# Kernel tuning notes

Measured on AMD Instinct MI355X. Metric: run time of the kernel, lower is better.

## Reference

```python
import jax, jax.numpy as jnp
import numpy as np

IN_F = 4096
OUT_F = 11008
GROUP_SIZE = 128
BITS = 4
PACK = 32 // BITS  # 8 uint4 nibbles per int32


def _unpack_uint4(packed):
    # packed: (rows, cols) int32 -> (rows, cols*8) int32 nibbles in [0,15]
    shifts = (jnp.arange(PACK, dtype=jnp.int32) * BITS)[None, None, :]
    nib = (packed[:, :, None] >> shifts) & 15
    return nib.reshape(packed.shape[0], packed.shape[1] * PACK)


def _dequant(qweight, qzeros, scales):
    # Mirrors torch.ops.hpu.convert_from_uint4: w = (uint4 - zp) * scale,
    # group-wise along the in_features dimension (rows).
    w = _unpack_uint4(qweight).astype(scales.dtype)          # (IN_F, OUT_F)
    zp = _unpack_uint4(qzeros).astype(scales.dtype)          # (n_groups, OUT_F)
    sc_full = jnp.repeat(scales, GROUP_SIZE, axis=0)          # (IN_F, OUT_F)
    zp_full = jnp.repeat(zp, GROUP_SIZE, axis=0)              # (IN_F, OUT_F)
    return (w - zp_full) * sc_full


def setup_inputs() -> dict:
    key = jax.random.key(0)
    k1, k2, k3, k4 = jax.random.split(key, 4)
    n_groups = IN_F // GROUP_SIZE
    inp = jax.random.normal(k1, (2, 2048, IN_F), dtype=jnp.float32)
    qweight = jax.random.randint(k2, (IN_F, OUT_F // PACK), 0, 2147483647, dtype=jnp.int32)
    qzeros = jax.random.randint(k3, (n_groups, OUT_F // PACK), 0, 2147483647, dtype=jnp.int32)
    scales = jax.random.uniform(k4, (n_groups, OUT_F), dtype=jnp.float32) * 0.01 + 1e-3
    return {"input": inp, "qweight": qweight, "qzeros": qzeros, "scales": scales}


def reference(input, qweight, qzeros, scales):
    weight = _dequant(qweight, qzeros, scales)                # (IN_F, OUT_F)
    out = jnp.einsum('bsi,io->bso', input, weight)            # (B, S, OUT_F)
    return out.astype(input.dtype)
```

## Files before the change

kernel.cpp:

```cpp
#include <hip/hip_runtime.h>
#include <stdint.h>

#define IN_F   4096
#define OUT_F  11008
#define QCOLS  (OUT_F / 8)
#define NGRP   32
#define M_TOT  4096

typedef __attribute__((ext_vector_type(8))) short short8;
typedef __attribute__((ext_vector_type(4))) float floatx4;

__device__ __forceinline__ short f2bf(float f) {
    union { float f; uint32_t u; } v; v.f = f;
    uint32_t u = v.u;
    u += 0x7FFFu + ((u >> 16) & 1u);
    return (short)(u >> 16);
}

__global__ __launch_bounds__(256)
void dequant_kernel(const int* __restrict__ qw, const int* __restrict__ qz,
                    const float* __restrict__ scl, short* __restrict__ wt)
{
    __shared__ int qlds[64 * 32];

    const int tid = threadIdx.x;
    const int nb  = blockIdx.x;
    const int kb  = blockIdx.y;
    const int n0  = nb * 256;
    const int c0  = nb * 32;
    const int k0  = kb * 64;
    const int g   = kb >> 1;

    #pragma unroll
    for (int i = 0; i < 8; ++i) {
        const int f = tid + i * 256;
        const int k = f >> 5, c = f & 31;
        qlds[f] = qw[(size_t)(k0 + k) * QCOLS + c0 + c];
    }
    __syncthreads();

    const int   cl = tid >> 3;
    const int   sh = (tid & 7) << 2;
    const uint32_t z  = (uint32_t)qz[(size_t)g * QCOLS + c0 + cl];
    const float sc = scl[(size_t)g * OUT_F + n0 + tid];
    const float zo = -(float)((z >> sh) & 15u) * sc;

    short8 o[8];
    #pragma unroll
    for (int i = 0; i < 8; ++i) {
        #pragma unroll
        for (int kk = 0; kk < 8; ++kk) {
            const uint32_t q = (uint32_t)qlds[(i * 8 + kk) * 32 + cl];
            o[i][kk] = f2bf(fmaf((float)((q >> sh) & 15u), sc, zo));
        }
    }

    short* dst = wt + (size_t)(n0 + tid) * IN_F + k0;
    #pragma unroll
    for (int i = 0; i < 8; ++i)
        *(short8*)(dst + i * 8) = o[i];
}

__global__ __launch_bounds__(256)
void cast_kernel(const float* __restrict__ A, short* __restrict__ Ab)
{
    const size_t i = ((size_t)blockIdx.x * 256 + threadIdx.x) * 8;
    const float4 a0 = *(const float4*)(A + i);
    const float4 a1 = *(const float4*)(A + i + 4);
    short8 o;
    o[0] = f2bf(a0.x); o[1] = f2bf(a0.y); o[2] = f2bf(a0.z); o[3] = f2bf(a0.w);
    o[4] = f2bf(a1.x); o[5] = f2bf(a1.y); o[6] = f2bf(a1.z); o[7] = f2bf(a1.w);
    *(short8*)(Ab + i) = o;
}

#define GBK 64

__global__ __launch_bounds__(256, 3)
void gemm_kernel(const short* __restrict__ Ab, const short* __restrict__ Bt,
                 float* __restrict__ out)
{
    __shared__ short As[128 * GBK];
    __shared__ short Bs[128 * GBK];

    const int tid  = threadIdx.x;
    const int lane = tid & 63;
    const int w    = tid >> 6;
    const int m0   = blockIdx.x * 128;
    const int n0   = blockIdx.y * 128;

    const int srow = lane >> 3;
    const int kseg = (lane & 7) ^ srow;
    const short* agp[4];
    const short* bgp[4];
    short* alp[4];
    short* blp[4];
    #pragma unroll
    for (int s = 0; s < 4; ++s) {
        const int slot = w * 4 + s;
        const int row  = slot * 8 + srow;
        agp[s] = Ab + (size_t)(m0 + row) * IN_F + kseg * 8;
        bgp[s] = Bt + (size_t)(n0 + row) * IN_F + kseg * 8;
        alp[s] = As + slot * 512;
        blp[s] = Bs + slot * 512;
    }

    const int lrow = lane & 15;
    const int quad = lane >> 4;
    const int wm   = ((w >> 1) & 1) << 6;
    const int wn   = (w & 1) << 6;

    int aoff[4], boff[4];
    #pragma unroll
    for (int i = 0; i < 4; ++i) {
        const int swz = (quad ^ (lrow & 7)) * 8;
        aoff[i] = (wm + i * 16 + lrow) * GBK + swz;
        boff[i] = (wn + i * 16 + lrow) * GBK + swz;
    }

    floatx4 acc[4][4];
    #pragma unroll
    for (int i = 0; i < 4; ++i)
        #pragma unroll
        for (int j = 0; j < 4; ++j)
            acc[i][j] = (floatx4)0.f;

    for (int it = 0; it < IN_F / GBK; ++it) {
        __syncthreads();
        #pragma unroll
        for (int s = 0; s < 4; ++s) {
            __builtin_amdgcn_global_load_lds(
                (const __attribute__((address_space(1))) void*)agp[s],
                (__attribute__((address_space(3))) void*)alp[s], 16, 0, 0);
            __builtin_amdgcn_global_load_lds(
                (const __attribute__((address_space(1))) void*)bgp[s],
                (__attribute__((address_space(3))) void*)blp[s], 16, 0, 0);
            agp[s] += GBK;
            bgp[s] += GBK;
        }
        __syncthreads();

        #pragma unroll
        for (int kx = 0; kx < 64; kx += 32) {
            short8 af[4], bf[4];
            #pragma unroll
            for (int mt = 0; mt < 4; ++mt)
                af[mt] = *(const short8*)(As + (aoff[mt] ^ kx));
            #pragma unroll
            for (int nt = 0; nt < 4; ++nt)
                bf[nt] = *(const short8*)(Bs + (boff[nt] ^ kx));
            #pragma unroll
            for (int mt = 0; mt < 4; ++mt)
                #pragma unroll
                for (int nt = 0; nt < 4; ++nt)
                    acc[mt][nt] = __builtin_amdgcn_mfma_f32_16x16x32_bf16(
                        af[mt], bf[nt], acc[mt][nt], 0, 0, 0);
        }
    }

    #pragma unroll
    for (int mt = 0; mt < 4; ++mt) {
        #pragma unroll
        for (int nt = 0; nt < 4; ++nt) {
            const int col = n0 + wn + nt * 16 + lrow;
            float* op = out + (size_t)(m0 + wm + mt * 16 + quad * 4) * OUT_F + col;
            #pragma unroll
            for (int r = 0; r < 4; ++r)
                op[(size_t)r * OUT_F] = acc[mt][nt][r];
        }
    }
}

#define BM 128
#define BN 128
#define LDA 40
#define LDB 40

__global__ __launch_bounds__(256, 2)
void wql_kernel(const float* __restrict__ A,
                const int*   __restrict__ qw,
                const int*   __restrict__ qz,
                const float* __restrict__ scl,
                float*       __restrict__ out)
{
    __shared__ short As[BM * LDA];
    __shared__ short Bs[BN * LDB];

    const int tid = threadIdx.x;
    const int m0  = blockIdx.y * BM;
    const int n0  = blockIdx.x * BN;

    const int a_row  = tid >> 1;
    const int a_kseg = (tid & 1) << 4;
    const float* a_base = A + (size_t)(m0 + a_row) * IN_F + a_kseg;
    short* a_wr = &As[a_row * LDA + a_kseg];

    const int b_n     = tid & 127;
    const int b_khalf = (tid >> 7) << 4;
    const int c_glob  = (n0 >> 3) + (b_n >> 3);
    const int shift   = (b_n & 7) << 2;
    short* b_wr = &Bs[b_n * LDB + b_khalf];

    const int lane = tid & 63;
    const int wm   = ((tid >> 7) & 1) << 6;
    const int wn   = ((tid >> 6) & 1) << 6;
    const int lrow = lane & 15;
    const int quad = lane >> 4;

    const short* a_rd = &As[(wm + lrow) * LDA + quad * 8];
    const short* b_rd = &Bs[(wn + lrow) * LDB + quad * 8];

    floatx4 acc[4][4];
    #pragma unroll
    for (int i = 0; i < 4; ++i)
        #pragma unroll
        for (int j = 0; j < 4; ++j)
            acc[i][j] = (floatx4)0.f;

    for (int g = 0; g < NGRP; ++g) {
        const uint32_t z  = (uint32_t)qz[g * QCOLS + c_glob];
        const float    sc = scl[g * OUT_F + n0 + b_n];
        const float    zo = -(float)((z >> shift) & 15u) * sc;

        #pragma unroll 1
        for (int t4 = 0; t4 < 4; ++t4) {
            const int k0 = (g << 7) + (t4 << 5);
            const float4* ap = (const float4*)(a_base + k0);
            float4 av0 = ap[0], av1 = ap[1], av2 = ap[2], av3 = ap[3];

            const int* qp = qw + (size_t)(k0 + b_khalf) * QCOLS + c_glob;
            uint32_t qv[16];
            #pragma unroll
            for (int kk = 0; kk < 16; ++kk) qv[kk] = (uint32_t)qp[kk * QCOLS];

            __syncthreads();

            short8 aw0, aw1;
            aw0[0]=f2bf(av0.x); aw0[1]=f2bf(av0.y); aw0[2]=f2bf(av0.z); aw0[3]=f2bf(av0.w);
            aw0[4]=f2bf(av1.x); aw0[5]=f2bf(av1.y); aw0[6]=f2bf(av1.z); aw0[7]=f2bf(av1.w);
            aw1[0]=f2bf(av2.x); aw1[1]=f2bf(av2.y); aw1[2]=f2bf(av2.z); aw1[3]=f2bf(av2.w);
            aw1[4]=f2bf(av3.x); aw1[5]=f2bf(av3.y); aw1[6]=f2bf(av3.z); aw1[7]=f2bf(av3.w);
            *(short8*)a_wr       = aw0;
            *(short8*)(a_wr + 8) = aw1;

            short8 bw0, bw1;
            #pragma unroll
            for (int kk = 0; kk < 8; ++kk)
                bw0[kk] = f2bf(fmaf((float)((qv[kk] >> shift) & 15u), sc, zo));
            #pragma unroll
            for (int kk = 0; kk < 8; ++kk)
                bw1[kk] = f2bf(fmaf((float)((qv[8 + kk] >> shift) & 15u), sc, zo));
            *(short8*)b_wr       = bw0;
            *(short8*)(b_wr + 8) = bw1;

            __syncthreads();

            short8 af[4], bf[4];
            #pragma unroll
            for (int mt = 0; mt < 4; ++mt)
                af[mt] = *(const short8*)(a_rd + mt * 16 * LDA);
            #pragma unroll
            for (int nt = 0; nt < 4; ++nt)
                bf[nt] = *(const short8*)(b_rd + nt * 16 * LDB);

            #pragma unroll
            for (int mt = 0; mt < 4; ++mt)
                #pragma unroll
                for (int nt = 0; nt < 4; ++nt)
                    acc[mt][nt] = __builtin_amdgcn_mfma_f32_16x16x32_bf16(
                        af[mt], bf[nt], acc[mt][nt], 0, 0, 0);
        }
    }

    #pragma unroll
    for (int mt = 0; mt < 4; ++mt) {
        #pragma unroll
        for (int nt = 0; nt < 4; ++nt) {
            const int col = n0 + wn + nt * 16 + lrow;
            float* op = out + (size_t)(m0 + wm + mt * 16 + quad * 4) * OUT_F + col;
            #pragma unroll
            for (int r = 0; r < 4; ++r)
                op[(size_t)r * OUT_F] = acc[mt][nt][r];
        }
    }
}

extern "C" void kernel_launch(void* const* d_in, const int* in_sizes, int n_in,
                              void* d_out, int out_size, void* d_ws, size_t ws_size,
                              hipStream_t stream) {
    const float* input   = (const float*)d_in[0];
    const int*   qweight = (const int*)d_in[1];
    const int*   qzeros  = (const int*)d_in[2];
    const float* scales  = (const float*)d_in[3];
    float*       out     = (float*)d_out;

    const size_t WT_BYTES = (size_t)OUT_F * IN_F * 2;
    const size_t AB_BYTES = (size_t)M_TOT * IN_F * 2;

    if (ws_size >= WT_BYTES + AB_BYTES) {
        short* wt = (short*)d_ws;
        short* ab = (short*)((char*)d_ws + WT_BYTES);

        dim3 dq_grid(OUT_F / 256, IN_F / 64);
        dequant_kernel<<<dq_grid, 256, 0, stream>>>(qweight, qzeros, scales, wt);
        cast_kernel<<<(size_t)M_TOT * IN_F / 8 / 256, 256, 0, stream>>>(input, ab);
        dim3 grid(M_TOT / 128, OUT_F / 128);
        gemm_kernel<<<grid, 256, 0, stream>>>(ab, wt, out);
    } else {
        dim3 grid(OUT_F / BN, M_TOT / BM);
        wql_kernel<<<grid, 256, 0, stream>>>(input, qweight, qzeros, scales, out);
    }
}
```

Measured before the change: 604.4 us.

## Replace GEMM with 256x256 double-buffered pipelined kernel and reshape dequant tiling

Replaces the 128x128 single-buffered bf16 MFMA GEMM with a 512-thread 256x256 tile kernel. It double-buffers LDS and interleaves async global-to-LDS loads with quarter-tile MFMA phases, using explicit waitcnt, barriers and s_setprio. This is meant to hide load latency and raise arithmetic intensity per block. The dequant kernel is retiled so each block covers 32 output columns by 512 K rows, with vectorised LDS reads and wider contiguous bf16 row writes. The trade-offs are much higher register and LDS pressure, fewer blocks (16x43), and fragile manual synchronisation.

Result: slower. 616.9 us (+2.1%).

```diff
diff --git a/kernel.cpp b/kernel.cpp
--- a/kernel.cpp
+++ b/kernel.cpp
@@ -21,44 +21,52 @@
 void dequant_kernel(const int* __restrict__ qw, const int* __restrict__ qz,
                     const float* __restrict__ scl, short* __restrict__ wt)
 {
-    __shared__ int qlds[64 * 32];
+    __shared__ int qt[4][520];
 
     const int tid = threadIdx.x;
     const int nb  = blockIdx.x;
     const int kb  = blockIdx.y;
-    const int n0  = nb * 256;
-    const int c0  = nb * 32;
-    const int k0  = kb * 64;
-    const int g   = kb >> 1;
+    const int n0  = nb * 32;
+    const int c0  = nb * 4;
+    const int k0  = kb * 512;
 
     #pragma unroll
     for (int i = 0; i < 8; ++i) {
         const int f = tid + i * 256;
-        const int k = f >> 5, c = f & 31;
-        qlds[f] = qw[(size_t)(k0 + k) * QCOLS + c0 + c];
+        qt[f & 3][f >> 2] = qw[(size_t)(k0 + (f >> 2)) * QCOLS + c0 + (f & 3)];
     }
     __syncthreads();
 
-    const int   cl = tid >> 3;
-    const int   sh = (tid & 7) << 2;
-    const uint32_t z  = (uint32_t)qz[(size_t)g * QCOLS + c0 + cl];
-    const float sc = scl[(size_t)g * OUT_F + n0 + tid];
-    const float zo = -(float)((z >> sh) & 15u) * sc;
-
-    short8 o[8];
-    #pragma unroll
-    for (int i = 0; i < 8; ++i) {
-        #pragma unroll
-        for (int kk = 0; kk < 8; ++kk) {
-            const uint32_t q = (uint32_t)qlds[(i * 8 + kk) * 32 + cl];
-            o[i][kk] = f2bf(fmaf((float)((q >> sh) & 15u), sc, zo));
+    const int n  = n0 + (tid >> 3);
+    const int cl = tid >> 6;
+    const int sh = (n & 7) << 2;
+    const int ks = (tid & 7) << 3;
+
+    short* dst = wt + (size_t)n * IN_F + k0 + ks;
+
+    #pragma unroll
+    for (int ip = 0; ip < 4; ++ip) {
+        const int g = kb * 4 + ip;
+        const uint32_t z  = (uint32_t)qz[(size_t)g * QCOLS + c0 + cl];
+        const float    sc = scl[(size_t)g * OUT_F + n];
+        const float    zo = -(float)((z >> sh) & 15u) * sc;
+        #pragma unroll
+        for (int ih = 0; ih < 2; ++ih) {
+            const int i = ip * 2 + ih;
+            const int4 q0 = *(const int4*)&qt[cl][i * 64 + ks];
+            const int4 q1 = *(const int4*)&qt[cl][i * 64 + ks + 4];
+            short8 o;
+            o[0] = f2bf(fmaf((float)(((uint32_t)q0.x >> sh) & 15u), sc, zo));
+            o[1] = f2bf(fmaf((float)(((uint32_t)q0.y >> sh) & 15u), sc, zo));
+            o[2] = f2bf(fmaf((float)(((uint32_t)q0.z >> sh) & 15u), sc, zo));
+            o[3] = f2bf(fmaf((float)(((uint32_t)q0.w >> sh) & 15u), sc, zo));
+            o[4] = f2bf(fmaf((float)(((uint32_t)q1.x >> sh) & 15u), sc, zo));
+            o[5] = f2bf(fmaf((float)(((uint32_t)q1.y >> sh) & 15u), sc, zo));
+            o[6] = f2bf(fmaf((float)(((uint32_t)q1.z >> sh) & 15u), sc, zo));
+            o[7] = f2bf(fmaf((float)(((uint32_t)q1.w >> sh) & 15u), sc, zo));
+            *(short8*)(dst + i * 64) = o;
         }
     }
-
-    short* dst = wt + (size_t)(n0 + tid) * IN_F + k0;
-    #pragma unroll
-    for (int i = 0; i < 8; ++i)
-        *(short8*)(dst + i * 8) = o[i];
 }
 
 __global__ __launch_bounds__(256)
@@ -73,96 +81,179 @@
     *(short8*)(Ab + i) = o;
 }
 
-#define GBK 64
-
-__global__ __launch_bounds__(256, 3)
-void gemm_kernel(const short* __restrict__ Ab, const short* __restrict__ Bt,
-                 float* __restrict__ out)
+#define GLL(src, dst) __builtin_amdgcn_global_load_lds(                        \
+    (const __attribute__((address_space(1))) void*)(src),                      \
+    (__attribute__((address_space(3))) void*)(dst), 16, 0, 0)
+
+#define BAR()  do { asm volatile("" ::: "memory");                             \
+                    __builtin_amdgcn_s_barrier();                              \
+                    asm volatile("" ::: "memory"); } while (0)
+
+__global__ __launch_bounds__(512, 2)
+void gemm256_kernel(const short* __restrict__ Ab, const short* __restrict__ Bt,
+                    float* __restrict__ out)
 {
-    __shared__ short As[128 * GBK];
-    __shared__ short Bs[128 * GBK];
+    __shared__ short As[2][2][8192];
+    __shared__ short Bs[2][2][8192];
 
     const int tid  = threadIdx.x;
     const int lane = tid & 63;
     const int w    = tid >> 6;
-    const int m0   = blockIdx.x * 128;
-    const int n0   = blockIdx.y * 128;
-
-    const int srow = lane >> 3;
-    const int kseg = (lane & 7) ^ srow;
-    const short* agp[4];
-    const short* bgp[4];
-    short* alp[4];
-    short* blp[4];
-    #pragma unroll
-    for (int s = 0; s < 4; ++s) {
-        const int slot = w * 4 + s;
-        const int row  = slot * 8 + srow;
-        agp[s] = Ab + (size_t)(m0 + row) * IN_F + kseg * 8;
-        bgp[s] = Bt + (size_t)(n0 + row) * IN_F + kseg * 8;
-        alp[s] = As + slot * 512;
-        blp[s] = Bs + slot * 512;
-    }
+    const int wm   = w >> 2;
+    const int wn   = w & 3;
+    const int m0   = blockIdx.x * 256;
+    const int n0   = blockIdx.y * 256;
+
+    const int r0 = tid >> 3;
+    const int sg = (((tid & 7) ^ (r0 & 7)) << 3);
+
+    const short* aS[2][2];
+    const short* bS[2][2];
+    aS[0][0] = Ab + (size_t)(m0 +       r0) * IN_F + sg;
+    aS[0][1] = Ab + (size_t)(m0 +  64 + r0) * IN_F + sg;
+    aS[1][0] = Ab + (size_t)(m0 + 128 + r0) * IN_F + sg;
+    aS[1][1] = Ab + (size_t)(m0 + 192 + r0) * IN_F + sg;
+    bS[0][0] = Bt + (size_t)(n0 +       r0) * IN_F + sg;
+    bS[0][1] = Bt + (size_t)(n0 +  64 + r0) * IN_F + sg;
+    bS[1][0] = Bt + (size_t)(n0 + 128 + r0) * IN_F + sg;
+    bS[1][1] = Bt + (size_t)(n0 + 192 + r0) * IN_F + sg;
+
+    const int ld0 = (tid - lane) << 3;
+    const int ld1 = 4096 + ld0;
 
     const int lrow = lane & 15;
     const int quad = lane >> 4;
-    const int wm   = ((w >> 1) & 1) << 6;
-    const int wn   = (w & 1) << 6;
-
-    int aoff[4], boff[4];
-    #pragma unroll
-    for (int i = 0; i < 4; ++i) {
-        const int swz = (quad ^ (lrow & 7)) * 8;
-        aoff[i] = (wm + i * 16 + lrow) * GBK + swz;
-        boff[i] = (wn + i * 16 + lrow) * GBK + swz;
-    }
-
-    floatx4 acc[4][4];
-    #pragma unroll
-    for (int i = 0; i < 4; ++i)
+    const int sw   = ((quad ^ (lrow & 7)) << 3);
+
+    int ao[8], bo[4];
+    #pragma unroll
+    for (int mt = 0; mt < 8; ++mt) ao[mt] = ((mt * 16 + lrow) << 6) + sw;
+    #pragma unroll
+    for (int nt = 0; nt < 4; ++nt)
+        bo[nt] = ((((wn & 1) << 6) + nt * 16 + lrow) << 6) + sw;
+
+    const short* Ard[2] = { &As[0][wm][0],      &As[1][wm][0] };
+    const short* Brd[2] = { &Bs[0][wn >> 1][0], &Bs[1][wn >> 1][0] };
+
+    floatx4 acc[8][4];
+    #pragma unroll
+    for (int i = 0; i < 8; ++i)
         #pragma unroll
         for (int j = 0; j < 4; ++j)
             acc[i][j] = (floatx4)0.f;
 
-    for (int it = 0; it < IN_F / GBK; ++it) {
-        __syncthreads();
-        #pragma unroll
-        for (int s = 0; s < 4; ++s) {
-            __builtin_amdgcn_global_load_lds(
-                (const __attribute__((address_space(1))) void*)agp[s],
-                (__attribute__((address_space(3))) void*)alp[s], 16, 0, 0);
-            __builtin_amdgcn_global_load_lds(
-                (const __attribute__((address_space(1))) void*)bgp[s],
-                (__attribute__((address_space(3))) void*)blp[s], 16, 0, 0);
-            agp[s] += GBK;
-            bgp[s] += GBK;
+    GLL(bS[0][0], &Bs[0][0][ld0]); GLL(bS[0][1], &Bs[0][0][ld1]);
+    GLL(bS[1][0], &Bs[0][1][ld0]); GLL(bS[1][1], &Bs[0][1][ld1]);
+    GLL(aS[0][0], &As[0][0][ld0]); GLL(aS[0][1], &As[0][0][ld1]);
+    GLL(aS[1][0], &As[0][1][ld0]); GLL(aS[1][1], &As[0][1][ld1]);
+    GLL(bS[0][0] + 64, &Bs[1][0][ld0]); GLL(bS[0][1] + 64, &Bs[1][0][ld1]);
+    GLL(bS[1][0] + 64, &Bs[1][1][ld0]); GLL(bS[1][1] + 64, &Bs[1][1][ld1]);
+    asm volatile("s_waitcnt vmcnt(4)" ::: "memory");
+    BAR();
+
+    short8 af[4][2], b01[2][2], b23[2][2];
+
+    for (int jj = 0; jj < 32; ++jj) {
+        #pragma unroll
+        for (int h = 0; h < 2; ++h) {
+            const int j  = jj * 2 + h;
+            const int kA = ((j + 1 < 64) ? j + 1 : 63) << 6;
+            const int kB = ((j + 2 < 64) ? j + 2 : 63) << 6;
+            const short* Ac = Ard[h];
+            const short* Bc = Brd[h];
+
+            #pragma unroll
+            for (int mt = 0; mt < 4; ++mt) {
+                af[mt][0] = *(const short8*)(Ac + ao[mt]);
+                af[mt][1] = *(const short8*)(Ac + (ao[mt] ^ 32));
+            }
+            #pragma unroll
+            for (int nt = 0; nt < 2; ++nt) {
+                b01[nt][0] = *(const short8*)(Bc + bo[nt]);
+                b01[nt][1] = *(const short8*)(Bc + (bo[nt] ^ 32));
+            }
+            GLL(aS[0][0] + kA, &As[h ^ 1][0][ld0]);
+            GLL(aS[0][1] + kA, &As[h ^ 1][0][ld1]);
+            BAR();
+            __builtin_amdgcn_s_setprio(1);
+            #pragma unroll
+            for (int kk = 0; kk < 2; ++kk)
+                #pragma unroll
+                for (int mt = 0; mt < 4; ++mt)
+                    #pragma unroll
+                    for (int nt = 0; nt < 2; ++nt)
+                        acc[mt][nt] = __builtin_amdgcn_mfma_f32_16x16x32_bf16(
+                            af[mt][kk], b01[nt][kk], acc[mt][nt], 0, 0, 0);
+            __builtin_amdgcn_s_setprio(0);
+            asm volatile("s_waitcnt lgkmcnt(0)" ::: "memory");
+            BAR();
+
+            #pragma unroll
+            for (int nt = 0; nt < 2; ++nt) {
+                b23[nt][0] = *(const short8*)(Bc + bo[nt + 2]);
+                b23[nt][1] = *(const short8*)(Bc + (bo[nt + 2] ^ 32));
+            }
+            GLL(aS[1][0] + kA, &As[h ^ 1][1][ld0]);
+            GLL(aS[1][1] + kA, &As[h ^ 1][1][ld1]);
+            BAR();
+            __builtin_amdgcn_s_setprio(1);
+            #pragma unroll
+            for (int kk = 0; kk < 2; ++kk)
+                #pragma unroll
+                for (int mt = 0; mt < 4; ++mt)
+                    #pragma unroll
+                    for (int nt = 0; nt < 2; ++nt)
+                        acc[mt][nt + 2] = __builtin_amdgcn_mfma_f32_16x16x32_bf16(
+                            af[mt][kk], b23[nt][kk], acc[mt][nt + 2], 0, 0, 0);
+            __builtin_amdgcn_s_setprio(0);
+            asm volatile("s_waitcnt lgkmcnt(0)" ::: "memory");
+            BAR();
+
+            #pragma unroll
+            for (int mt = 0; mt < 4; ++mt) {
+                af[mt][0] = *(const short8*)(Ac + ao[mt + 4]);
+                af[mt][1] = *(const short8*)(Ac + (ao[mt + 4] ^ 32));
+            }
+            GLL(bS[0][0] + kB, &Bs[h][0][ld0]);
+            GLL(bS[0][1] + kB, &Bs[h][0][ld1]);
+            BAR();
+            __builtin_amdgcn_s_setprio(1);
+            #pragma unroll
+            for (int kk = 0; kk < 2; ++kk)
+                #pragma unroll
+                for (int mt = 0; mt < 4; ++mt)
+                    #pragma unroll
+                    for (int nt = 0; nt < 2; ++nt)
+                        acc[mt + 4][nt + 2] = __builtin_amdgcn_mfma_f32_16x16x32_bf16(
+                            af[mt][kk], b23[nt][kk], acc[mt + 4][nt + 2], 0, 0, 0);
+            __builtin_amdgcn_s_setprio(0);
+            asm volatile("s_waitcnt lgkmcnt(0)" ::: "memory");
+            BAR();
+
+            GLL(bS[1][0] + kB, &Bs[h][1][ld0]);
+            GLL(bS[1][1] + kB, &Bs[h][1][ld1]);
+            BAR();
+            __builtin_amdgcn_s_setprio(1);
+            #pragma unroll
+            for (int kk = 0; kk < 2; ++kk)
+                #pragma unroll
+                for (int mt = 0; mt < 4; ++mt)
+                    #pragma unroll
+                    for (int nt = 0; nt < 2; ++nt)
+                        acc[mt + 4][nt] = __builtin_amdgcn_mfma_f32_16x16x32_bf16(
+                            af[mt][kk], b01[nt][kk], acc[mt + 4][nt], 0, 0, 0);
+            __builtin_amdgcn_s_setprio(0);
+            asm volatile("s_waitcnt vmcnt(4)" ::: "memory");
+            BAR();
         }
-        __syncthreads();
-
-        #pragma unroll
-        for (int kx = 0; kx < 64; kx += 32) {
-            short8 af[4], bf[4];
-            #pragma unroll
-            for (int mt = 0; mt < 4; ++mt)
-                af[mt] = *(const short8*)(As + (aoff[mt] ^ kx));
-            #pragma unroll
-            for (int nt = 0; nt < 4; ++nt)
-                bf[nt] = *(const short8*)(Bs + (boff[nt] ^ kx));
-            #pragma unroll
-            for (int mt = 0; mt < 4; ++mt)
-                #pragma unroll
-                for (int nt = 0; nt < 4; ++nt)
-                    acc[mt][nt] = __builtin_amdgcn_mfma_f32_16x16x32_bf16(
-                        af[mt], bf[nt], acc[mt][nt], 0, 0, 0);
-        }
-    }
-
-    #pragma unroll
-    for (int mt = 0; mt < 4; ++mt) {
+    }
+
+    #pragma unroll
+    for (int mt = 0; mt < 8; ++mt) {
         #pragma unroll
         for (int nt = 0; nt < 4; ++nt) {
-            const int col = n0 + wn + nt * 16 + lrow;
-            float* op = out + (size_t)(m0 + wm + mt * 16 + quad * 4) * OUT_F + col;
+            const int col = n0 + (wn << 6) + nt * 16 + lrow;
+            float* op = out + (size_t)(m0 + (wm << 7) + mt * 16 + (quad << 2)) * OUT_F + col;
             #pragma unroll
             for (int r = 0; r < 4; ++r)
                 op[(size_t)r * OUT_F] = acc[mt][nt][r];
@@ -300,11 +391,11 @@
         short* wt = (short*)d_ws;
         short* ab = (short*)((char*)d_ws + WT_BYTES);
 
-        dim3 dq_grid(OUT_F / 256, IN_F / 64);
+        dim3 dq_grid(OUT_F / 32, IN_F / 512);
         dequant_kernel<<<dq_grid, 256, 0, stream>>>(qweight, qzeros, scales, wt);
         cast_kernel<<<(size_t)M_TOT * IN_F / 8 / 256, 256, 0, stream>>>(input, ab);
-        dim3 grid(M_TOT / 128, OUT_F / 128);
-        gemm_kernel<<<grid, 256, 0, stream>>>(ab, wt, out);
+        dim3 grid(M_TOT / 256, OUT_F / 256);
+        gemm256_kernel<<<grid, 512, 0, stream>>>(ab, wt, out);
     } else {
         dim3 grid(OUT_F / BN, M_TOT / BM);
         wql_kernel<<<grid, 256, 0, stream>>>(input, qweight, qzeros, scales, out);
```

## Fuse cast and dequant into one prep kernel, swizzle GEMM block order

Applied to the files above, without the earlier changes.

Merges the input cast and weight dequantization into a single launch so the two prep phases share one grid and avoid a kernel boundary. The dequant path is restructured so each block covers 32 output rows by 512 K, with each thread writing contiguous 64-element K runs from a transposed LDS tile. The GEMM grid becomes 1D with a block-index swizzle over 8 slices, which changes the order tiles are visited and is meant to improve L2 reuse of A/B tiles. This adds index arithmetic and relies on the hardcoded 344/32 tile counts.

After: 663.7 us. 9.8% more time.

```diff
diff --git a/kernel.cpp b/kernel.cpp
--- a/kernel.cpp
+++ b/kernel.cpp
@@ -17,60 +17,74 @@
     return (short)(u >> 16);
 }
 
+#define CAST_BLOCKS 8192
+#define DQ_BLOCKS   (344 * 8)
+
 __global__ __launch_bounds__(256)
-void dequant_kernel(const int* __restrict__ qw, const int* __restrict__ qz,
-                    const float* __restrict__ scl, short* __restrict__ wt)
+void prep_kernel(const float* __restrict__ A, short* __restrict__ Ab,
+                 const int* __restrict__ qw, const int* __restrict__ qz,
+                 const float* __restrict__ scl, short* __restrict__ wt)
 {
-    __shared__ int qlds[64 * 32];
+    __shared__ int qt[4][520];
 
     const int tid = threadIdx.x;
-    const int nb  = blockIdx.x;
-    const int kb  = blockIdx.y;
-    const int n0  = nb * 256;
-    const int c0  = nb * 32;
-    const int k0  = kb * 64;
-    const int g   = kb >> 1;
+    const int bx  = blockIdx.x;
+
+    if (bx < CAST_BLOCKS) {
+        const size_t i = ((size_t)bx * 256 + tid) * 8;
+        const float4 a0 = *(const float4*)(A + i);
+        const float4 a1 = *(const float4*)(A + i + 4);
+        short8 o;
+        o[0] = f2bf(a0.x); o[1] = f2bf(a0.y); o[2] = f2bf(a0.z); o[3] = f2bf(a0.w);
+        o[4] = f2bf(a1.x); o[5] = f2bf(a1.y); o[6] = f2bf(a1.z); o[7] = f2bf(a1.w);
+        *(short8*)(Ab + i) = o;
+        return;
+    }
+
+    const int db = bx - CAST_BLOCKS;
+    const int nb = db % 344;
+    const int kb = db / 344;
+    const int n0 = nb * 32;
+    const int c0 = nb * 4;
+    const int k0 = kb * 512;
 
     #pragma unroll
     for (int i = 0; i < 8; ++i) {
         const int f = tid + i * 256;
-        const int k = f >> 5, c = f & 31;
-        qlds[f] = qw[(size_t)(k0 + k) * QCOLS + c0 + c];
+        qt[f & 3][f >> 2] = qw[(size_t)(k0 + (f >> 2)) * QCOLS + c0 + (f & 3)];
     }
     __syncthreads();
 
-    const int   cl = tid >> 3;
-    const int   sh = (tid & 7) << 2;
-    const uint32_t z  = (uint32_t)qz[(size_t)g * QCOLS + c0 + cl];
-    const float sc = scl[(size_t)g * OUT_F + n0 + tid];
-    const float zo = -(float)((z >> sh) & 15u) * sc;
-
-    short8 o[8];
-    #pragma unroll
-    for (int i = 0; i < 8; ++i) {
-        #pragma unroll
-        for (int kk = 0; kk < 8; ++kk) {
-            const uint32_t q = (uint32_t)qlds[(i * 8 + kk) * 32 + cl];
-            o[i][kk] = f2bf(fmaf((float)((q >> sh) & 15u), sc, zo));
-        }
-    }
-
-    short* dst = wt + (size_t)(n0 + tid) * IN_F + k0;
-    #pragma unroll
-    for (int i = 0; i < 8; ++i)
-        *(short8*)(dst + i * 8) = o[i];
-}
-
-__global__ __launch_bounds__(256)
-void cast_kernel(const float* __restrict__ A, short* __restrict__ Ab)
-{
-    const size_t i = ((size_t)blockIdx.x * 256 + threadIdx.x) * 8;
-    const float4 a0 = *(const float4*)(A + i);
-    const float4 a1 = *(const float4*)(A + i + 4);
-    short8 o;
-    o[0] = f2bf(a0.x); o[1] = f2bf(a0.y); o[2] = f2bf(a0.z); o[3] = f2bf(a0.w);
-    o[4] = f2bf(a1.x); o[5] = f2bf(a1.y); o[6] = f2bf(a1.z); o[7] = f2bf(a1.w);
-    *(short8*)(Ab + i) = o;
+    const int n  = n0 + (tid >> 3);
+    const int cl = tid >> 6;
+    const int sh = (n & 7) << 2;
+    const int ks = (tid & 7) << 3;
+
+    short* dst = wt + (size_t)n * IN_F + k0 + ks;
+
+    #pragma unroll
+    for (int ip = 0; ip < 4; ++ip) {
+        const int g = kb * 4 + ip;
+        const uint32_t z  = (uint32_t)qz[(size_t)g * QCOLS + c0 + cl];
+        const float    sc = scl[(size_t)g * OUT_F + n];
+        const float    zo = -(float)((z >> sh) & 15u) * sc;
+        #pragma unroll
+        for (int ih = 0; ih < 2; ++ih) {
+            const int i = ip * 2 + ih;
+            const int4 q0 = *(const int4*)&qt[cl][i * 64 + ks];
+            const int4 q1 = *(const int4*)&qt[cl][i * 64 + ks + 4];
+            short8 o;
+            o[0] = f2bf(fmaf((float)(((uint32_t)q0.x >> sh) & 15u), sc, zo));
+            o[1] = f2bf(fmaf((float)(((uint32_t)q0.y >> sh) & 15u), sc, zo));
+            o[2] = f2bf(fmaf((float)(((uint32_t)q0.z >> sh) & 15u), sc, zo));
+            o[3] = f2bf(fmaf((float)(((uint32_t)q0.w >> sh) & 15u), sc, zo));
+            o[4] = f2bf(fmaf((float)(((uint32_t)q1.x >> sh) & 15u), sc, zo));
+            o[5] = f2bf(fmaf((float)(((uint32_t)q1.y >> sh) & 15u), sc, zo));
+            o[6] = f2bf(fmaf((float)(((uint32_t)q1.z >> sh) & 15u), sc, zo));
+            o[7] = f2bf(fmaf((float)(((uint32_t)q1.w >> sh) & 15u), sc, zo));
+            *(short8*)(dst + i * 64) = o;
+        }
+    }
 }
 
 #define GBK 64
@@ -85,8 +99,11 @@
     const int tid  = threadIdx.x;
     const int lane = tid & 63;
     const int w    = tid >> 6;
-    const int m0   = blockIdx.x * 128;
-    const int n0   = blockIdx.y * 128;
+
+    const int lin = blockIdx.x;
+    const int swz = (lin & 7) * 344 + (lin >> 3);
+    const int m0  = (swz & 31) << 7;
+    const int n0  = (swz >> 5) << 7;
 
     const int srow = lane >> 3;
     const int kseg = (lane & 7) ^ srow;
@@ -112,9 +129,9 @@
     int aoff[4], boff[4];
     #pragma unroll
     for (int i = 0; i < 4; ++i) {
-        const int swz = (quad ^ (lrow & 7)) * 8;
-        aoff[i] = (wm + i * 16 + lrow) * GBK + swz;
-        boff[i] = (wn + i * 16 + lrow) * GBK + swz;
+        const int swl = (quad ^ (lrow & 7)) * 8;
+        aoff[i] = (wm + i * 16 + lrow) * GBK + swl;
+        boff[i] = (wn + i * 16 + lrow) * GBK + swl;
     }
 
     floatx4 acc[4][4];
@@ -300,11 +317,9 @@
         short* wt = (short*)d_ws;
         short* ab = (short*)((char*)d_ws + WT_BYTES);
 
-        dim3 dq_grid(OUT_F / 256, IN_F / 64);
-        dequant_kernel<<<dq_grid, 256, 0, stream>>>(qweight, qzeros, scales, wt);
-        cast_kernel<<<(size_t)M_TOT * IN_F / 8 / 256, 256, 0, stream>>>(input, ab);
-        dim3 grid(M_TOT / 128, OUT_F / 128);
-        gemm_kernel<<<grid, 256, 0, stream>>>(ab, wt, out);
+        prep_kernel<<<CAST_BLOCKS + DQ_BLOCKS, 256, 0, stream>>>(
+            input, ab, qweight, qzeros, scales, wt);
+        gemm_kernel<<<2752, 256, 0, stream>>>(ab, wt, out);
     } else {
         dim3 grid(OUT_F / BN, M_TOT / BM);
         wql_kernel<<<grid, 256, 0, stream>>>(input, qweight, qzeros, scales, out);
```
